# Performance work log

Measured on AMD Instinct MI355X. Metric: run time of the kernel, lower is better.

## Reference

```python
import jax, jax.numpy as jnp
import numpy as np

D_MODEL = 512
NUM_HEADS = 8
QUERY_GROUPS = 2
HEAD_DIM = D_MODEL // NUM_HEADS  # 64
ROPE_THETA = 10000.0
SCALE = 0.125  # 1/sqrt(head_dim)
NEG_INF = -1e9


def setup_inputs() -> dict:
    key = jax.random.key(0)
    k1, k2, k3 = jax.random.split(key, 3)
    B, T, S = 2, 512, 16
    x = jax.random.normal(k1, (B, T, S, D_MODEL), jnp.float32)
    padding_mask = jnp.ones((B, T * S), jnp.int32)  # [B, T*H*W], all valid
    qkv_dim = NUM_HEADS * HEAD_DIM + 2 * QUERY_GROUPS * HEAD_DIM  # 768
    qkv_w = jax.random.normal(k2, (qkv_dim, D_MODEL), jnp.float32) / np.float32(np.sqrt(D_MODEL))
    o_w = jax.random.normal(k3, (D_MODEL, NUM_HEADS * HEAD_DIM), jnp.float32) / np.float32(np.sqrt(D_MODEL))
    return {"x": x, "padding_mask": padding_mask, "qkv_w": qkv_w, "o_w": o_w}


def _rope(v, pos):
    # v: [N, T, h, d]; classic RoPE (rotate-half) over temporal positions
    half = v.shape[-1] // 2
    inv_freq = 1.0 / (ROPE_THETA ** (jnp.arange(0, half, dtype=jnp.float32) / half))
    ang = pos[:, None] * inv_freq  # [T, half]
    cos = jnp.cos(ang)[None, :, None, :]
    sin = jnp.sin(ang)[None, :, None, :]
    v1, v2 = v[..., :half], v[..., half:]
    return jnp.concatenate([v1 * cos - v2 * sin, v1 * sin + v2 * cos], axis=-1)


def reference(x, padding_mask, qkv_w, o_w):
    B, T, S, D = x.shape
    # temporal attention: flatten spatial patches into batch -> [B*S, T, D]
    xt = x.transpose(0, 2, 1, 3).reshape(B * S, T, D)
    qkv = xt @ qkv_w.T  # [B*S, T, (H+2G)*hd]
    q_end = NUM_HEADS * HEAD_DIM
    k_end = q_end + QUERY_GROUPS * HEAD_DIM
    q = qkv[..., :q_end].reshape(B * S, T, NUM_HEADS, HEAD_DIM)
    k = qkv[..., q_end:k_end].reshape(B * S, T, QUERY_GROUPS, HEAD_DIM)
    v = qkv[..., k_end:].reshape(B * S, T, QUERY_GROUPS, HEAD_DIM)
    pos = jnp.arange(T, dtype=jnp.float32)
    q = _rope(q, pos)
    k = _rope(k, pos)
    # GQA: broadcast each KV group to its query heads
    rep = NUM_HEADS // QUERY_GROUPS
    k = jnp.repeat(k, rep, axis=2)
    v = jnp.repeat(v, rep, axis=2)
    scores = jnp.einsum('nqhd,nkhd->nhqk', q, k) * SCALE  # [B*S, H, T, T]
    causal = jnp.tril(jnp.ones((T, T), bool))
    pm = padding_mask.astype(bool).reshape(-1, T)  # [B*S, T] query-side mask (as in torch path)
    mask = causal[None, None, :, :] & pm[:, None, :, None]
    scores = jnp.where(mask, scores, NEG_INF)
    attn = jax.nn.softmax(scores, axis=-1)
    out = jnp.einsum('nhqk,nkhd->nqhd', attn, v).reshape(B * S, T, D)
    out = out @ o_w.T  # output projection
    return out.reshape(B, S, T, D).transpose(0, 2, 1, 3)  # back to [B, T, S, D]
```

## Files before the change

### kernel.cpp

```cpp
#include <hip/hip_runtime.h>
#include <hip/hip_bf16.h>

typedef __attribute__((ext_vector_type(8))) short bf16x8;
typedef __attribute__((ext_vector_type(4))) float f32x4;
typedef __attribute__((ext_vector_type(4))) short s16x4;

#define DM 512
#define T_SEQ 512
#define NSEQ 32
#define MROWS 16384
#define QKV_DIM 768
#define HD 64
#define NEG_INF_F (-1000000000.0f)
#define LOG2E 1.44269504088896340736f

__device__ __forceinline__ short f2bf(float f) {
    unsigned int u = __builtin_bit_cast(unsigned int, f);
    unsigned int r = (u + 0x7FFFu + ((u >> 16) & 1u)) >> 16;
    return (short)r;
}

__device__ __forceinline__ short f2bf_hw(float f) {
    __hip_bfloat16 h = __float2bfloat16(f);
    return __builtin_bit_cast(short, h);
}

__device__ __forceinline__ void gload16(const void* g, void* l) {
    __builtin_amdgcn_global_load_lds(
        (const __attribute__((address_space(1))) void*)g,
        (__attribute__((address_space(3))) void*)l, 16, 0, 0);
}

__global__ __launch_bounds__(128) void k_convert(
    const float* __restrict__ x, const float* __restrict__ qkvw, const float* __restrict__ owf,
    short* __restrict__ xt, short* __restrict__ qw, short* __restrict__ ow,
    float* __restrict__ cosT, float* __restrict__ sinT)
{
    int bidx = blockIdx.x, tid = threadIdx.x;
    if (bidx < MROWS) {
        int m = bidx; int n = m >> 9, t = m & 511, b = n >> 4, s = n & 15;
        const float* src = x + ((size_t)((b * 512 + t) * 16 + s)) * 512;
        float4 v = *(const float4*)(src + tid * 4);
        s16x4 o; o.x = f2bf(v.x); o.y = f2bf(v.y); o.z = f2bf(v.z); o.w = f2bf(v.w);
        *(s16x4*)(xt + (size_t)m * 512 + tid * 4) = o;
    } else if (bidx < MROWS + 1280) {
        int wr = bidx - MROWS;
        const float* src; short* dst;
        if (wr < QKV_DIM) { src = qkvw + (size_t)wr * 512; dst = qw + (size_t)wr * 512; }
        else             { src = owf + (size_t)(wr - QKV_DIM) * 512; dst = ow + (size_t)(wr - QKV_DIM) * 512; }
        float4 v = *(const float4*)(src + tid * 4);
        s16x4 o; o.x = f2bf(v.x); o.y = f2bf(v.y); o.z = f2bf(v.z); o.w = f2bf(v.w);
        *(s16x4*)(dst + tid * 4) = o;
    } else {
        int idx = (bidx - (MROWS + 1280)) * 128 + tid;
        int t = idx >> 5, d = idx & 31;
        float inv = powf(10000.0f, -(float)d * (1.0f / 32.0f));
        float ang = (float)t * inv;
        float sv, cv; sincosf(ang, &sv, &cv);
        cosT[idx] = cv; sinT[idx] = sv;
    }
}

__device__ __forceinline__ void gemm_mainloop_db(
    const short* __restrict__ Ab, const short* __restrict__ Bb, int K,
    short* As0, short* As1, short* Bs0, short* Bs1,
    int wave, int lane, f32x4 acc[4][4])
{
    int wr = (wave >> 1) * 64, wc = (wave & 1) * 64;
    int cl = lane & 15, g = lane >> 4;
    auto stg = [&](int kt, short* As, short* Bs) {
        #pragma unroll
        for (int c = 0; c < 2; ++c) {
            int chunk = (wave * 2 + c) * 64 + lane;
            int row = chunk >> 2, kc = chunk & 3;
            gload16(Ab + (size_t)row * K + kt + kc * 8, As + (wave * 2 + c) * 512);
            gload16(Bb + (size_t)row * K + kt + kc * 8, Bs + (wave * 2 + c) * 512);
        }
    };
    stg(0, As0, Bs0);
    for (int kt = 0; kt < K; kt += 32) {
        short* Asc = (kt & 32) ? As1 : As0;
        short* Bsc = (kt & 32) ? Bs1 : Bs0;
        short* Asn = (kt & 32) ? As0 : As1;
        short* Bsn = (kt & 32) ? Bs0 : Bs1;
        __syncthreads();
        if (kt + 32 < K) stg(kt + 32, Asn, Bsn);
        bf16x8 af[4], bg[4];
        #pragma unroll
        for (int mf = 0; mf < 4; ++mf)
            af[mf] = *(const bf16x8*)(Asc + (wr + mf * 16 + cl) * 32 + (g << 3));
        #pragma unroll
        for (int nf = 0; nf < 4; ++nf)
            bg[nf] = *(const bf16x8*)(Bsc + (wc + nf * 16 + cl) * 32 + (g << 3));
        #pragma unroll
        for (int mf = 0; mf < 4; ++mf)
            #pragma unroll
            for (int nf = 0; nf < 4; ++nf)
                acc[mf][nf] = __builtin_amdgcn_mfma_f32_16x16x32_bf16(af[mf], bg[nf], acc[mf][nf], 0, 0, 0);
    }
}

__global__ __launch_bounds__(256) void k_gemm_qkv(
    const short* __restrict__ xt, const short* __restrict__ qw,
    const float* __restrict__ cosT, const float* __restrict__ sinT,
    short* __restrict__ qb, short* __restrict__ kb, short* __restrict__ vtb)
{
    __shared__ short As0[128 * 32], As1[128 * 32], Bs0[128 * 32], Bs1[128 * 32];
    __shared__ short Vld[4][16 * 64];
    int tid = threadIdx.x, wave = tid >> 6, lane = tid & 63;
    int cl = lane & 15, g = lane >> 4;
    int bm = blockIdx.x, bn = blockIdx.y;
    f32x4 acc[4][4] = {};
    gemm_mainloop_db(xt + (size_t)bm * 128 * 512, qw + (size_t)bn * 128 * 512, 512,
                     As0, As1, Bs0, Bs1, wave, lane, acc);

    const float QSC = 0.125f * LOG2E;
    int wr = (wave >> 1) * 64, wc = (wave & 1) * 64;
    int gbase = bn * 128 + wc;

    if (gbase < 640) {
        #pragma unroll
        for (int mf = 0; mf < 4; ++mf) {
            #pragma unroll
            for (int rg = 0; rg < 4; ++rg) {
                int r = bm * 128 + wr + mf * 16 + (g << 2) + rg;
                int n = r >> 9, t = r & 511;
                #pragma unroll
                for (int nf = 0; nf < 2; ++nf) {
                    int dlo = nf * 16 + cl;
                    float v1 = acc[mf][nf][rg];
                    float v2 = acc[mf][nf + 2][rg];
                    float c = cosT[t * 32 + dlo], s = sinT[t * 32 + dlo];
                    if (gbase < 512) {
                        int h = gbase >> 6;
                        size_t base = ((size_t)(n * 8 + h) * 512 + t) * 64;
                        qb[base + dlo]      = f2bf_hw((v1 * c - v2 * s) * QSC);
                        qb[base + dlo + 32] = f2bf_hw((v1 * s + v2 * c) * QSC);
                    } else {
                        int gk = (gbase - 512) >> 6;
                        size_t base = ((size_t)(n * 2 + gk) * 512 + t) * 64;
                        kb[base + dlo]      = f2bf_hw(v1 * c - v2 * s);
                        kb[base + dlo + 32] = f2bf_hw(v1 * s + v2 * c);
                    }
                }
            }
        }
    } else {
        int gq = (gbase - 640) >> 6;
        #pragma unroll
        for (int mf = 0; mf < 4; ++mf) {
            #pragma unroll
            for (int nf = 0; nf < 2; ++nf) {
                int dlo = nf * 16 + cl;
                s16x4 plo, phi;
                #pragma unroll
                for (int rg = 0; rg < 4; ++rg) {
                    ((short*)&plo)[rg] = f2bf_hw(acc[mf][nf][rg]);
                    ((short*)&phi)[rg] = f2bf_hw(acc[mf][nf + 2][rg]);
                }
                *(s16x4*)(&Vld[wave][dlo * 16 + (g << 2)])        = plo;
                *(s16x4*)(&Vld[wave][(dlo + 32) * 16 + (g << 2)]) = phi;
            }
            int r0 = bm * 128 + wr + mf * 16;
            int n = r0 >> 9, t0 = r0 & 511;
            size_t vb = ((size_t)(n * 2 + gq) * 64 + lane) * 512;
            bf16x8 va = *(const bf16x8*)(&Vld[wave][lane * 16]);
            bf16x8 vb8 = *(const bf16x8*)(&Vld[wave][lane * 16 + 8]);
            *(bf16x8*)(vtb + vb + t0)     = va;
            *(bf16x8*)(vtb + vb + t0 + 8) = vb8;
        }
    }
}

__global__ __launch_bounds__(256) void k_attn(
    const short* __restrict__ qb, const short* __restrict__ kb, const short* __restrict__ vtb,
    const int* __restrict__ pm, short* __restrict__ ao)
{
    __shared__ short Kt[2][64 * 64];
    __shared__ short Vt[2][64 * 64];
    __shared__ short Pws[4][16 * 64];
    int tid = threadIdx.x, wave = tid >> 6, lane = tid & 63;
    int cl = lane & 15, g = lane >> 4;
    int bid = blockIdx.x;
    int c = bid & 3, h = (bid >> 2) & 7, n = bid >> 5;
    int kg = h >> 2;
    const short* Qb = qb + ((size_t)(n * 8 + h) * 512) * 64;
    const short* Kb = kb + ((size_t)(n * 2 + kg) * 512) * 64;
    const short* Vb = vtb + ((size_t)(n * 2 + kg) * 64) * 512;

    auto stage = [&](int jt, int buf) {
        int c0 = jt * 64;
        #pragma unroll
        for (int cc = 0; cc < 2; ++cc) {
            int chunk = (wave * 2 + cc) * 64 + lane;
            int row = chunk >> 3, kc = chunk & 7;
            int sw = (kc ^ (row & 7)) << 3;
            gload16(Kb + (size_t)(c0 + row) * 64 + sw, &Kt[buf][(wave * 2 + cc) * 512]);
            gload16(Vb + (size_t)row * 512 + c0 + sw, &Vt[buf][(wave * 2 + cc) * 512]);
        }
    };

    stage(0, 0);
    int buf = 0;
    #pragma unroll
    for (int ph = 0; ph < 2; ++ph) {
        int rowb = (ph ? (7 - c) : c) * 64 + wave * 16;
        int NTp = ph ? (8 - c) : (c + 1);
        bf16x8 qf[2];
        #pragma unroll
        for (int ks = 0; ks < 2; ++ks)
            qf[ks] = *(const bf16x8*)(Qb + (size_t)(rowb + cl) * 64 + ks * 32 + (g << 3));
        f32x4 Oc[4] = {};
        float mrow = -1e30f, lrow = 0.f;
        bool rv = pm[n * 512 + rowb + cl] != 0;
        int rq = rowb + cl;

        for (int jt = 0; jt < NTp; ++jt) {
            __syncthreads();
            if (jt + 1 < NTp) stage(jt + 1, buf ^ 1);
            else if (ph == 0) stage(0, buf ^ 1);
            int c0 = jt * 64;
            const short* Kc = Kt[buf];
            const short* Vc = Vt[buf];
            buf ^= 1;

            f32x4 sacc[4] = {};
            #pragma unroll
            for (int ks = 0; ks < 2; ++ks) {
                #pragma unroll
                for (int nf = 0; nf < 4; ++nf) {
                    int row = nf * 16 + cl;
                    int kc = ks * 4 + g;
                    bf16x8 kf = *(const bf16x8*)(Kc + row * 64 + ((kc ^ (row & 7)) << 3));
                    sacc[nf] = __builtin_amdgcn_mfma_f32_16x16x32_bf16(kf, qf[ks], sacc[nf], 0, 0, 0);
                }
            }

            const bool diag = (jt == NTp - 1);
            float rmax = -1e30f;
            if (diag) {
                #pragma unroll
                for (int nf = 0; nf < 4; ++nf)
                    #pragma unroll
                    for (int rg = 0; rg < 4; ++rg) {
                        int kv = c0 + nf * 16 + g * 4 + rg;
                        float sv = sacc[nf][rg];
                        sv = (kv <= rq && rv) ? sv : NEG_INF_F;
                        sacc[nf][rg] = sv;
                        rmax = fmaxf(rmax, sv);
                    }
            } else {
                #pragma unroll
                for (int nf = 0; nf < 4; ++nf)
                    #pragma unroll
                    for (int rg = 0; rg < 4; ++rg)
                        rmax = fmaxf(rmax, sacc[nf][rg]);
            }
            rmax = fmaxf(rmax, __shfl_xor(rmax, 16));
            rmax = fmaxf(rmax, __shfl_xor(rmax, 32));
            float mold = mrow;
            int defer = __all(rmax - mold <= 8.0f);
            float mnew = defer ? mold : fmaxf(mold, rmax);
            mrow = mnew;
            float rsum = 0.f;
            #pragma unroll
            for (int nf = 0; nf < 4; ++nf) {
                s16x4 pk;
                #pragma unroll
                for (int rg = 0; rg < 4; ++rg) {
                    float p = exp2f(sacc[nf][rg] - mnew);
                    rsum += p;
                    ((short*)&pk)[rg] = f2bf_hw(p);
                }
                *(s16x4*)(&Pws[wave][cl * 64 + ((((nf << 1) + (g >> 1)) ^ (cl & 7)) << 3) + ((g & 1) << 2)]) = pk;
            }
            rsum += __shfl_xor(rsum, 16);
            rsum += __shfl_xor(rsum, 32);
            if (defer) {
                lrow += rsum;
            } else {
                float alpha = exp2f(mold - mnew);
                lrow = lrow * alpha + rsum;
                #pragma unroll
                for (int rg = 0; rg < 4; ++rg) {
                    float av = __shfl(alpha, (lane & 48) + (g << 2) + rg);
                    #pragma unroll
                    for (int nf = 0; nf < 4; ++nf) Oc[nf][rg] *= av;
                }
            }

            #pragma unroll
            for (int ks = 0; ks < 2; ++ks) {
                bf16x8 pf = *(const bf16x8*)(&Pws[wave][cl * 64 + (((ks * 4 + g) ^ (cl & 7)) << 3)]);
                #pragma unroll
                for (int nf = 0; nf < 4; ++nf) {
                    int row = nf * 16 + cl;
                    int kc = ks * 4 + g;
                    bf16x8 vf = *(const bf16x8*)(Vc + row * 64 + ((kc ^ (row & 7)) << 3));
                    Oc[nf] = __builtin_amdgcn_mfma_f32_16x16x32_bf16(pf, vf, Oc[nf], 0, 0, 0);
                }
            }
        }

        #pragma unroll
        for (int rg = 0; rg < 4; ++rg) {
            float li = __shfl(lrow, (lane & 48) + (g << 2) + rg);
            float inv = 1.0f / li;
            int r = rowb + g * 4 + rg;
            size_t base = ((size_t)n * 512 + r) * 512 + h * 64;
            #pragma unroll
            for (int nf = 0; nf < 4; ++nf)
                ao[base + nf * 16 + cl] = f2bf_hw(Oc[nf][rg] * inv);
        }
    }
}

__global__ __launch_bounds__(256) void k_gemm_out(
    const short* __restrict__ ao, const short* __restrict__ ow, float* __restrict__ out)
{
    __shared__ short As0[128 * 32], As1[128 * 32], Bs0[128 * 32], Bs1[128 * 32];
    int tid = threadIdx.x, wave = tid >> 6, lane = tid & 63;
    int bm = blockIdx.x, bn = blockIdx.y;
    f32x4 acc[4][4] = {};
    gemm_mainloop_db(ao + (size_t)bm * 128 * 512, ow + (size_t)bn * 128 * 512, 512,
                     As0, As1, Bs0, Bs1, wave, lane, acc);

    int wr = (wave >> 1) * 64, wc = (wave & 1) * 64;
    #pragma unroll
    for (int mf = 0; mf < 4; ++mf) {
        #pragma unroll
        for (int rg = 0; rg < 4; ++rg) {
            int r = bm * 128 + wr + mf * 16 + ((lane >> 4) << 2) + rg;
            int n = r >> 9, t = r & 511, b = n >> 4, s = n & 15;
            size_t obase = ((size_t)((b * 512 + t) * 16 + s)) * 512;
            #pragma unroll
            for (int nf = 0; nf < 4; ++nf) {
                int ccc = bn * 128 + wc + nf * 16 + (lane & 15);
                out[obase + ccc] = acc[mf][nf][rg];
            }
        }
    }
}

extern "C" void kernel_launch(void* const* d_in, const int* in_sizes, int n_in,
                              void* d_out, int out_size, void* d_ws, size_t ws_size,
                              hipStream_t stream) {
    (void)in_sizes; (void)n_in; (void)out_size; (void)ws_size;
    const float* x    = (const float*)d_in[0];
    const int*   pmsk = (const int*)d_in[1];
    const float* qkvw = (const float*)d_in[2];
    const float* owf  = (const float*)d_in[3];
    char* ws = (char*)d_ws;
    short* xt   = (short*)(ws + 0);
    short* qw   = (short*)(ws + 16777216);
    short* ow   = (short*)(ws + 17563648);
    float* cosT = (float*)(ws + 18087936);
    float* sinT = (float*)(ws + 18153472);
    short* qbuf = (short*)(ws + 18219008);
    short* kbuf = (short*)(ws + 34996224);
    short* vtbuf= (short*)(ws + 39190528);
    short* aobuf = xt;
    float* out = (float*)d_out;

    k_convert<<<dim3(17792), dim3(128), 0, stream>>>(x, qkvw, owf, xt, qw, ow, cosT, sinT);
    k_gemm_qkv<<<dim3(128, 6), dim3(256), 0, stream>>>(xt, qw, cosT, sinT, qbuf, kbuf, vtbuf);
    k_attn<<<dim3(1024), dim3(256), 0, stream>>>(qbuf, kbuf, vtbuf, pmsk, aobuf);
    k_gemm_out<<<dim3(128, 4), dim3(256), 0, stream>>>(aobuf, ow, out);
}
```

Baseline: 84.30 us.

## Fuse x transpose and bf16 conversion into QKV GEMM A-tile staging

Removes the separate pass that transposed and converted x (32 MB fp32 read, 16 MB bf16 write) into a bf16 buffer. The QKV GEMM now loads fp32 x rows directly with the transposed indexing, converts them to bf16 in registers and stores them to LDS. The B operand keeps its async global-to-LDS loads. In exchange, each of the 6 column blocks re-reads fp32 x (twice the bytes of bf16), and the A loads become synchronous register loads that are less overlapped with the MFMA work.

```diff
diff --git a/kernel.cpp b/kernel.cpp
--- a/kernel.cpp
+++ b/kernel.cpp
@@ -32,19 +32,13 @@
 }
 
 __global__ __launch_bounds__(128) void k_convert(
-    const float* __restrict__ x, const float* __restrict__ qkvw, const float* __restrict__ owf,
-    short* __restrict__ xt, short* __restrict__ qw, short* __restrict__ ow,
+    const float* __restrict__ qkvw, const float* __restrict__ owf,
+    short* __restrict__ qw, short* __restrict__ ow,
     float* __restrict__ cosT, float* __restrict__ sinT)
 {
     int bidx = blockIdx.x, tid = threadIdx.x;
-    if (bidx < MROWS) {
-        int m = bidx; int n = m >> 9, t = m & 511, b = n >> 4, s = n & 15;
-        const float* src = x + ((size_t)((b * 512 + t) * 16 + s)) * 512;
-        float4 v = *(const float4*)(src + tid * 4);
-        s16x4 o; o.x = f2bf(v.x); o.y = f2bf(v.y); o.z = f2bf(v.z); o.w = f2bf(v.w);
-        *(s16x4*)(xt + (size_t)m * 512 + tid * 4) = o;
-    } else if (bidx < MROWS + 1280) {
-        int wr = bidx - MROWS;
+    if (bidx < 1280) {
+        int wr = bidx;
         const float* src; short* dst;
         if (wr < QKV_DIM) { src = qkvw + (size_t)wr * 512; dst = qw + (size_t)wr * 512; }
         else             { src = owf + (size_t)(wr - QKV_DIM) * 512; dst = ow + (size_t)(wr - QKV_DIM) * 512; }
@@ -52,7 +46,7 @@
         s16x4 o; o.x = f2bf(v.x); o.y = f2bf(v.y); o.z = f2bf(v.z); o.w = f2bf(v.w);
         *(s16x4*)(dst + tid * 4) = o;
     } else {
-        int idx = (bidx - (MROWS + 1280)) * 128 + tid;
+        int idx = (bidx - 1280) * 128 + tid;
         int t = idx >> 5, d = idx & 31;
         float inv = powf(10000.0f, -(float)d * (1.0f / 32.0f));
         float ang = (float)t * inv;
@@ -101,7 +95,7 @@
 }
 
 __global__ __launch_bounds__(256) void k_gemm_qkv(
-    const short* __restrict__ xt, const short* __restrict__ qw,
+    const float* __restrict__ x, const short* __restrict__ qw,
     const float* __restrict__ cosT, const float* __restrict__ sinT,
     short* __restrict__ qb, short* __restrict__ kb, short* __restrict__ vtb)
 {
@@ -110,12 +104,63 @@
     int tid = threadIdx.x, wave = tid >> 6, lane = tid & 63;
     int cl = lane & 15, g = lane >> 4;
     int bm = blockIdx.x, bn = blockIdx.y;
+    const short* Bb = qw + (size_t)bn * 128 * 512;
+
+    const float* xrowp[2];
+    int choff[2];
+    #pragma unroll
+    for (int c = 0; c < 2; ++c) {
+        int chunk = (wave * 2 + c) * 64 + lane;
+        int row = chunk >> 2, kc = chunk & 3;
+        int m = bm * 128 + row, n = m >> 9, t = m & 511, b = n >> 4, s = n & 15;
+        xrowp[c] = x + ((size_t)((b * 512 + t) * 16 + s)) * 512 + kc * 8;
+        choff[c] = chunk * 8;
+    }
+    auto stgA = [&](int kt, short* As) {
+        #pragma unroll
+        for (int c = 0; c < 2; ++c) {
+            float4 fa = *(const float4*)(xrowp[c] + kt);
+            float4 fb = *(const float4*)(xrowp[c] + kt + 4);
+            bf16x8 v;
+            v[0] = f2bf_hw(fa.x); v[1] = f2bf_hw(fa.y); v[2] = f2bf_hw(fa.z); v[3] = f2bf_hw(fa.w);
+            v[4] = f2bf_hw(fb.x); v[5] = f2bf_hw(fb.y); v[6] = f2bf_hw(fb.z); v[7] = f2bf_hw(fb.w);
+            *(bf16x8*)(As + choff[c]) = v;
+        }
+    };
+    auto stgB = [&](int kt, short* Bs) {
+        #pragma unroll
+        for (int c = 0; c < 2; ++c) {
+            int chunk = (wave * 2 + c) * 64 + lane;
+            int row = chunk >> 2, kc = chunk & 3;
+            gload16(Bb + (size_t)row * 512 + kt + kc * 8, Bs + (wave * 2 + c) * 512);
+        }
+    };
+
+    int wr = (wave >> 1) * 64, wc = (wave & 1) * 64;
     f32x4 acc[4][4] = {};
-    gemm_mainloop_db(xt + (size_t)bm * 128 * 512, qw + (size_t)bn * 128 * 512, 512,
-                     As0, As1, Bs0, Bs1, wave, lane, acc);
+    stgB(0, Bs0); stgA(0, As0);
+    for (int kt = 0; kt < 512; kt += 32) {
+        short* Asc = (kt & 32) ? As1 : As0;
+        short* Bsc = (kt & 32) ? Bs1 : Bs0;
+        short* Asn = (kt & 32) ? As0 : As1;
+        short* Bsn = (kt & 32) ? Bs0 : Bs1;
+        __syncthreads();
+        if (kt + 32 < 512) { stgB(kt + 32, Bsn); stgA(kt + 32, Asn); }
+        bf16x8 af[4], bg[4];
+        #pragma unroll
+        for (int mf = 0; mf < 4; ++mf)
+            af[mf] = *(const bf16x8*)(Asc + (wr + mf * 16 + cl) * 32 + (g << 3));
+        #pragma unroll
+        for (int nf = 0; nf < 4; ++nf)
+            bg[nf] = *(const bf16x8*)(Bsc + (wc + nf * 16 + cl) * 32 + (g << 3));
+        #pragma unroll
+        for (int mf = 0; mf < 4; ++mf)
+            #pragma unroll
+            for (int nf = 0; nf < 4; ++nf)
+                acc[mf][nf] = __builtin_amdgcn_mfma_f32_16x16x32_bf16(af[mf], bg[nf], acc[mf][nf], 0, 0, 0);
+    }
 
     const float QSC = 0.125f * LOG2E;
-    int wr = (wave >> 1) * 64, wc = (wave & 1) * 64;
     int gbase = bn * 128 + wc;
 
     if (gbase < 640) {
@@ -351,7 +396,7 @@
     const float* qkvw = (const float*)d_in[2];
     const float* owf  = (const float*)d_in[3];
     char* ws = (char*)d_ws;
-    short* xt   = (short*)(ws + 0);
+    short* aobuf= (short*)(ws + 0);
     short* qw   = (short*)(ws + 16777216);
     short* ow   = (short*)(ws + 17563648);
     float* cosT = (float*)(ws + 18087936);
@@ -359,11 +404,10 @@
     short* qbuf = (short*)(ws + 18219008);
     short* kbuf = (short*)(ws + 34996224);
     short* vtbuf= (short*)(ws + 39190528);
-    short* aobuf = xt;
     float* out = (float*)d_out;
 
-    k_convert<<<dim3(17792), dim3(128), 0, stream>>>(x, qkvw, owf, xt, qw, ow, cosT, sinT);
-    k_gemm_qkv<<<dim3(128, 6), dim3(256), 0, stream>>>(xt, qw, cosT, sinT, qbuf, kbuf, vtbuf);
+    k_convert<<<dim3(1408), dim3(128), 0, stream>>>(qkvw, owf, qw, ow, cosT, sinT);
+    k_gemm_qkv<<<dim3(128, 6), dim3(256), 0, stream>>>(x, qw, cosT, sinT, qbuf, kbuf, vtbuf);
     k_attn<<<dim3(1024), dim3(256), 0, stream>>>(qbuf, kbuf, vtbuf, pmsk, aobuf);
     k_gemm_out<<<dim3(128, 4), dim3(256), 0, stream>>>(aobuf, ow, out);
 }
```

After: 102.1 us. 1.21x slower.
